# Optimization experiments

Measured on AMD Instinct MI355X. Metric: run time of the kernel, lower is better.

## Reference

```python
import jax, jax.numpy as jnp
import numpy as np

_SAMPLING_EPS = 1e-5


def setup_inputs() -> dict:
    key = jax.random.key(0)
    k1, k2, k3, k4, k5, k6 = jax.random.split(key, 6)
    B, V = 128, 128000
    return {
        "logits": jax.random.normal(k1, (B, V), dtype=jnp.float32),
        "temperature": jax.random.uniform(k2, (B,), dtype=jnp.float32),
        "min_p": jax.random.uniform(k3, (B,), dtype=jnp.float32),
        "top_k": jax.random.randint(k4, (B,), 0, 1024),
        "top_p": jax.random.uniform(k5, (B,), dtype=jnp.float32),
        "q": jax.random.uniform(k6, (B, V), dtype=jnp.float32),
        "num_logprobs": 20,
    }


def reference(logits, temperature, min_p, top_k, top_p, q, num_logprobs):
    B, V = logits.shape
    # raw logprobs computed BEFORE any processing (as in Sampler.forward)
    raw_logprobs = jax.nn.log_softmax(logits, axis=-1)
    # greedy sample on unscaled logits
    greedy = jnp.argmax(logits, axis=-1)
    # temperature scaling
    lt = logits / temperature[:, None]
    # min-p filtering
    probs = jax.nn.softmax(lt, axis=-1)
    max_p = jnp.max(probs, axis=-1, keepdims=True)
    lt = jnp.where(probs >= min_p[:, None] * max_p, lt, -jnp.inf)
    # top-k / top-p filtering on ascending-sorted logits (vLLM style)
    idx = jnp.argsort(lt, axis=-1)                       # ascending
    ls = jnp.take_along_axis(lt, idx, axis=-1)
    k = jnp.clip(top_k, 1, V)
    kth = jnp.take_along_axis(ls, (V - k)[:, None], axis=-1)  # k-th largest value
    ls = jnp.where(ls < kth, -jnp.inf, ls)
    ps = jax.nn.softmax(ls, axis=-1)
    csum = jnp.cumsum(ps, axis=-1)
    pmask = csum <= (1.0 - top_p)[:, None]
    pmask = pmask.at[:, -1].set(False)                   # always keep the max token
    ls = jnp.where(pmask, -jnp.inf, ls)
    inv = jnp.argsort(idx, axis=-1)                      # inverse permutation (scatter back)
    filtered = jnp.take_along_axis(ls, inv, axis=-1)
    # exponential-race sampling: argmax(probs / Exp(1)) ~ Categorical(probs)
    probs2 = jax.nn.softmax(filtered, axis=-1)
    expo = -jnp.log(jnp.clip(q, 1e-10, 1.0))
    rand_sampled = jnp.argmax(probs2 / expo, axis=-1)
    sampled = jnp.where(temperature < _SAMPLING_EPS, greedy, rand_sampled)
    # gather_logprobs: top-k logprobs + sampled-token logprob + rank
    topk_lp, topk_idx = jax.lax.top_k(raw_logprobs, num_logprobs)
    tok_lp = jnp.take_along_axis(raw_logprobs, sampled[:, None], axis=-1)  # (B,1)
    ranks = jnp.sum(raw_logprobs >= tok_lp, axis=-1)
    out_idx = jnp.concatenate([sampled[:, None], topk_idx], axis=1).astype(jnp.int32)
    out_lp = jnp.concatenate([tok_lp, topk_lp], axis=1)  # (B, num_logprobs+1)
    return (sampled[:, None].astype(jnp.int32), out_idx, out_lp, ranks)
```

## Files before the change

kernel.cpp:

```cpp
#include <hip/hip_runtime.h>
#include <math.h>

#define NB 1024
#define C_CAP 2048
#define BLK1 512
#define BLK2 1024
#define LCAP2 2048
#define FLOORB 682
#define BIN_SCALE ((float)NB / 12.0f)
#define BOUND 1.9921875f

__device__ __forceinline__ int bin_of(float x) {
  int b = (int)floorf((x + 6.0f) * BIN_SCALE);
  return min(max(b, 0), NB - 1);
}
__device__ __forceinline__ unsigned long long pack_vi(float v, int idx) {
  return ((unsigned long long)__float_as_uint(v) << 32) | (unsigned int)idx;
}
__device__ __forceinline__ unsigned long long okey(float v, int idx) {
  unsigned int u = __float_as_uint(v);
  u = (u & 0x80000000u) ? ~u : (u | 0x80000000u);
  return ((unsigned long long)u << 32) | (unsigned long long)(0x7fffffffu - (unsigned int)idx);
}
__device__ __forceinline__ float okey_val(unsigned long long k) {
  unsigned int hi = (unsigned int)(k >> 32);
  unsigned int u = (hi & 0x80000000u) ? (hi & 0x7fffffffu) : ~hi;
  return __uint_as_float(u);
}
__device__ __forceinline__ int okey_idx(unsigned long long k) {
  return (int)(0x7fffffffu - (unsigned int)k);
}

__global__ __launch_bounds__(BLK1)
void k1_scan(const float* __restrict__ logits, int V, int halfElems,
             unsigned long long* __restrict__ plist, int* __restrict__ pcnt,
             float* __restrict__ psum) {
  const int row = blockIdx.y, half = blockIdx.x, tid = threadIdx.x;
  const int lane = tid & 63;
  const float* lrow = logits + (size_t)row * V;
  const int start = half * halfElems;
  const int end = min(start + halfElems, V);
  __shared__ unsigned long long lst[LCAP2];
  __shared__ float rs[BLK1];
  __shared__ int lcnt;
  if (tid == 0) lcnt = 0;
  __syncthreads();
  float sum = 0.0f;
  const int n = max(end - start, 0);
  const int n4 = n >> 2;
  const float4* p4 = (const float4*)(lrow + start);
  int i = tid;
  for (; i + BLK1 < n4; i += 2 * BLK1) {
    float4 a = p4[i], b2 = p4[i + BLK1];
    float va[8] = {a.x, a.y, a.z, a.w, b2.x, b2.y, b2.z, b2.w};
    int ia[8];
    #pragma unroll
    for (int c2 = 0; c2 < 4; c2++) { ia[c2] = (i << 2) + c2; ia[c2 + 4] = ((i + BLK1) << 2) + c2; }
    #pragma unroll
    for (int c2 = 0; c2 < 8; c2++) {
      float x = va[c2];
      sum += __expf(fminf(x, 70.0f) - 6.0f);
      bool pred = (x >= BOUND);
      unsigned long long mk = __ballot(pred);
      if (mk) {
        int leader = __ffsll((long long)mk) - 1;
        int base = 0;
        if (lane == leader) base = atomicAdd(&lcnt, __popcll(mk));
        base = __shfl(base, leader, 64);
        if (pred) {
          int p = base + __popcll(mk & ((1ull << lane) - 1ull));
          if (p < LCAP2) lst[p] = pack_vi(x, start + ia[c2]);
        }
      }
    }
  }
  for (; i < n4; i += BLK1) {
    float4 a = p4[i];
    float va[4] = {a.x, a.y, a.z, a.w};
    #pragma unroll
    for (int c2 = 0; c2 < 4; c2++) {
      float x = va[c2];
      sum += __expf(fminf(x, 70.0f) - 6.0f);
      bool pred = (x >= BOUND);
      unsigned long long mk = __ballot(pred);
      if (mk) {
        int leader = __ffsll((long long)mk) - 1;
        int base = 0;
        if (lane == leader) base = atomicAdd(&lcnt, __popcll(mk));
        base = __shfl(base, leader, 64);
        if (pred) {
          int p = base + __popcll(mk & ((1ull << lane) - 1ull));
          if (p < LCAP2) lst[p] = pack_vi(x, start + (i << 2) + c2);
        }
      }
    }
  }
  for (int j = (n4 << 2) + tid; j < n; j += BLK1) {
    float x = lrow[start + j];
    sum += __expf(fminf(x, 70.0f) - 6.0f);
    bool pred = (x >= BOUND);
    unsigned long long mk = __ballot(pred);
    if (mk) {
      int leader = __ffsll((long long)mk) - 1;
      int base = 0;
      if (lane == leader) base = atomicAdd(&lcnt, __popcll(mk));
      base = __shfl(base, leader, 64);
      if (pred) {
        int p = base + __popcll(mk & ((1ull << lane) - 1ull));
        if (p < LCAP2) lst[p] = pack_vi(x, start + j);
      }
    }
  }
  __syncthreads();
  rs[tid] = sum;
  __syncthreads();
  for (int s = BLK1 / 2; s > 0; s >>= 1) {
    if (tid < s) rs[tid] += rs[tid + s];
    __syncthreads();
  }
  const size_t rc = (size_t)row * 2 + half;
  if (tid == 0) { psum[rc] = rs[0]; pcnt[rc] = lcnt; }
  int m = min(lcnt, LCAP2);
  unsigned long long* prow = plist + rc * LCAP2;
  for (int j = tid; j < m; j += BLK1) prow[j] = lst[j];
}

__global__ __launch_bounds__(BLK2)
void k2_fused(const float* __restrict__ logits,
              const float* __restrict__ temperature,
              const float* __restrict__ min_p,
              const int* __restrict__ top_k,
              const float* __restrict__ top_p,
              const float* __restrict__ q,
              const int* __restrict__ nl_ptr,
              int V, int B,
              const unsigned long long* __restrict__ plist,
              const int* __restrict__ pcnt,
              const float* __restrict__ psum,
              float* __restrict__ out) {
  const int row = blockIdx.x, tid = threadIdx.x;
  __shared__ int h[NB + 1];
  __shared__ int cur[NB];
  __shared__ unsigned long long lst[2 * LCAP2];
  __shared__ unsigned long long bkt[C_CAP];
  __shared__ float sv[C_CAP];
  __shared__ int   si[C_CAP];
  __shared__ float ss[C_CAP];
  __shared__ float st[BLK2];
  __shared__ float rf[BLK2], rf2[BLK2];
  __shared__ int   ri[BLK2];
  __shared__ int   s_fail, s_b;
  __shared__ float s_lse;

  for (int i = tid; i < NB; i += BLK2) { h[i] = 0; cur[i] = 0; }
  if (tid == 0) { s_b = 0; h[NB] = 0; }
  __syncthreads();

  const int p0 = pcnt[(size_t)row * 2], p1 = pcnt[(size_t)row * 2 + 1];
  const int c0 = min(p0, LCAP2), c1 = min(p1, LCAP2);
  const int tot = c0 + c1;
  int nl = nl_ptr[0];
  int ke = top_k[row]; ke = min(max(ke, 1), V);
  const int Kp = max(ke, nl);
  const bool fast = (p0 <= LCAP2) && (p1 <= LCAP2) && (tot >= Kp);

  if (tid == 0) s_lse = 6.0f + logf(psum[(size_t)row * 2] + psum[(size_t)row * 2 + 1]);

  const float* lrow = logits + (size_t)row * V;
  const int n4 = V >> 2;
  const float4* p4 = (const float4*)lrow;

  if (fast) {
    const unsigned long long* pr0 = plist + (size_t)row * 2 * LCAP2;
    const unsigned long long* pr1 = pr0 + LCAP2;
    for (int j = tid; j < c0; j += BLK2) lst[j] = pr0[j];
    for (int j = tid; j < c1; j += BLK2) lst[c0 + j] = pr1[j];
    __syncthreads();
    for (int j = tid; j < tot; j += BLK2) {
      float x = __uint_as_float((unsigned int)(lst[j] >> 32));
      atomicAdd(&h[bin_of(x)], 1);
    }
  } else {
    for (int ii = tid; ii < n4; ii += BLK2) {
      float4 a4 = p4[ii];
      atomicAdd(&h[bin_of(a4.x)], 1); atomicAdd(&h[bin_of(a4.y)], 1);
      atomicAdd(&h[bin_of(a4.z)], 1); atomicAdd(&h[bin_of(a4.w)], 1);
    }
    for (int j = (n4 << 2) + tid; j < V; j += BLK2)
      atomicAdd(&h[bin_of(lrow[j])], 1);
  }
  __syncthreads();

  for (int off = 1; off < NB; off <<= 1) {
    int t0 = (tid + off < NB) ? h[tid + off] : 0;
    __syncthreads();
    h[tid] += t0;
    __syncthreads();
  }
  if (h[tid] >= Kp) atomicMax(&s_b, tid);
  __syncthreads();
  const int bstar = s_b;
  int c = min(h[bstar], C_CAP); if (c < 1) c = 1;

  if (fast) {
    for (int j = tid; j < tot; j += BLK2) {
      unsigned long long kk = lst[j];
      float x = __uint_as_float((unsigned int)(kk >> 32));
      int idx = (int)(unsigned int)kk;
      int b = bin_of(x);
      if (b >= bstar) {
        int a = atomicAdd(&cur[b], 1);
        int pos = h[b + 1] + a;
        if (pos < C_CAP) bkt[pos] = okey(x, idx);
      }
    }
  } else {
    for (int ii = tid; ii < n4; ii += BLK2) {
      float4 a4 = p4[ii];
      float va[4] = {a4.x, a4.y, a4.z, a4.w};
      #pragma unroll
      for (int c2 = 0; c2 < 4; c2++) {
        int b = bin_of(va[c2]);
        if (b >= bstar) {
          int a = atomicAdd(&cur[b], 1);
          int pos = h[b + 1] + a;
          if (pos < C_CAP) bkt[pos] = okey(va[c2], (ii << 2) + c2);
        }
      }
    }
    for (int j = (n4 << 2) + tid; j < V; j += BLK2) {
      float x = lrow[j];
      int b = bin_of(x);
      if (b >= bstar) {
        int a = atomicAdd(&cur[b], 1);
        int pos = h[b + 1] + a;
        if (pos < C_CAP) bkt[pos] = okey(x, j);
      }
    }
  }
  __syncthreads();

  for (int pos = tid; pos < c; pos += BLK2) {
    unsigned long long k0 = bkt[pos];
    float v = okey_val(k0);
    int b = bin_of(v);
    int gs = h[b + 1];
    int ge = min(h[b], c);
    int rk = 0;
    for (int j = gs; j < ge; j++) if (bkt[j] > k0) rk++;
    int fin = gs + rk;
    sv[fin] = v; si[fin] = okey_idx(k0);
  }
  __syncthreads();

  float temp = temperature[row];
  bool ug = (temp < 1e-5f);
  float rt = 1.0f / (ug ? 1.0f : temp);
  float mp = min_p[row], tp = top_p[row];
  ke = min(ke, c);
  float v0 = sv[0];
  float lt0 = v0 * rt;

  float ltk = sv[ke - 1] * rt;
  float kth = (expf(ltk - lt0) >= mp) ? ltk : -INFINITY;

  if (tid == 0) s_fail = c;
  __syncthreads();
  for (int ii = tid; ii < c; ii += BLK2) {
    float ltj = sv[ii] * rt;
    if (!((expf(ltj - lt0) >= mp) && (ltj >= kth))) { atomicMin(&s_fail, ii); break; }
  }
  __syncthreads();
  int n1 = s_fail; if (n1 < 1) n1 = 1;
  __syncthreads();

  int L = (c + BLK2 - 1) / BLK2;
  int base = tid * L;
  int lim = min(base + L, c);
  float run = 0.0f;
  for (int j = base; j < lim; j++) {
    float pj = (j < n1) ? expf(sv[j] * rt - lt0) : 0.0f;
    run += pj; ss[j] = run;
  }
  st[tid] = run;
  __syncthreads();
  for (int off = 1; off < BLK2; off <<= 1) {
    float t0 = (tid >= off) ? st[tid - off] : 0.0f;
    __syncthreads();
    st[tid] += t0;
    __syncthreads();
  }
  float offv = (tid > 0) ? st[tid - 1] : 0.0f;
  for (int j = base; j < lim; j++) ss[j] += offv;
  __syncthreads();
  float Z1 = ss[n1 - 1];

  if (tid == 0) s_fail = n1;
  __syncthreads();
  for (int ii = tid; ii < n1; ii += BLK2) {
    if (ii > 0 && !((1.0f - ss[ii - 1] / Z1) > (1.0f - tp))) { atomicMin(&s_fail, ii); break; }
  }
  __syncthreads();
  int n2 = s_fail; if (n2 < 1) n2 = 1;
  __syncthreads();
  float Z2 = ss[n2 - 1];

  const float* qrow = q + (size_t)row * V;
  float bsc = -INFINITY; int bidx = 0x7fffffff; float bval = 0.0f;
  for (int ii = tid; ii < n2; ii += BLK2) {
    float pj = expf(sv[ii] * rt - lt0);
    float qv = qrow[si[ii]];
    qv = fminf(fmaxf(qv, 1e-10f), 1.0f);
    float sc = (pj / Z2) / (-logf(qv));
    if (sc > bsc || (sc == bsc && si[ii] < bidx)) { bsc = sc; bidx = si[ii]; bval = sv[ii]; }
  }
  rf[tid] = bsc; ri[tid] = bidx; rf2[tid] = bval;
  __syncthreads();
  for (int s = BLK2 / 2; s > 0; s >>= 1) {
    if (tid < s) {
      if (rf[tid + s] > rf[tid] ||
          (rf[tid + s] == rf[tid] && ri[tid + s] < ri[tid])) {
        rf[tid] = rf[tid + s]; ri[tid] = ri[tid + s]; rf2[tid] = rf2[tid + s];
      }
    }
    __syncthreads();
  }
  int sampled = ug ? si[0] : ri[0];
  float val_s = ug ? sv[0] : rf2[0];
  float lse = s_lse;
  float tok_lp = val_s - lse;
  __syncthreads();

  if (tid == 0) s_fail = c;
  __syncthreads();
  for (int ii = tid; ii < c; ii += BLK2)
    if (!((sv[ii] - lse) >= tok_lp)) { atomicMin(&s_fail, ii); break; }
  __syncthreads();
  int rank = s_fail;

  int W = nl + 1;
  if (tid == 0) {
    out[row] = (float)sampled;
    out[B + row * W] = (float)sampled;
    out[B + B * W + row * W] = tok_lp;
    out[B + 2 * B * W + row] = (float)rank;
  }
  for (int t = tid; t < nl; t += BLK2) {
    out[B + row * W + 1 + t] = (float)si[t];
    out[B + B * W + row * W + 1 + t] = sv[t] - lse;
  }
}

extern "C" void kernel_launch(void* const* d_in, const int* in_sizes, int n_in,
                              void* d_out, int out_size, void* d_ws, size_t ws_size,
                              hipStream_t stream) {
  const float* logits      = (const float*)d_in[0];
  const float* temperature = (const float*)d_in[1];
  const float* min_p       = (const float*)d_in[2];
  const int*   top_k       = (const int*)d_in[3];
  const float* top_p       = (const float*)d_in[4];
  const float* q           = (const float*)d_in[5];
  const int*   nl_ptr      = (const int*)d_in[6];

  int B = in_sizes[1];
  int V = in_sizes[0] / B;
  float* out = (float*)d_out;
  int halfElems = (((V + 1) / 2) + 3) & ~3;

  unsigned char* w = (unsigned char*)d_ws;
  unsigned long long* plist = (unsigned long long*)w; w += (size_t)B * 2 * LCAP2 * sizeof(unsigned long long);
  int* pcnt = (int*)w;                                w += (size_t)B * 2 * sizeof(int);
  float* psum = (float*)w;                            w += (size_t)B * 2 * sizeof(float);

  hipLaunchKernelGGL(k1_scan, dim3(2, B), dim3(BLK1), 0, stream,
                     logits, V, halfElems, plist, pcnt, psum);
  hipLaunchKernelGGL(k2_fused, dim3(B), dim3(BLK2), 0, stream,
                     logits, temperature, min_p, top_k, top_p, q, nl_ptr,
                     V, B, plist, pcnt, psum, out);
}
```

Before: 174.5 us.

## Use per-wave candidate segments and shuffle reductions in scan; halve fused block size

```diff
diff --git a/kernel.cpp b/kernel.cpp
--- a/kernel.cpp
+++ b/kernel.cpp
@@ -4,7 +4,9 @@
 #define NB 1024
 #define C_CAP 2048
 #define BLK1 512
-#define BLK2 1024
+#define BLK2 512
+#define NWAVES1 (BLK1 / 64)
+#define WSEG 512
 #define LCAP2 2048
 #define FLOORB 682
 #define BIN_SCALE ((float)NB / 12.0f)
@@ -36,41 +38,36 @@
              unsigned long long* __restrict__ plist, int* __restrict__ pcnt,
              float* __restrict__ psum) {
   const int row = blockIdx.y, half = blockIdx.x, tid = threadIdx.x;
-  const int lane = tid & 63;
+  const int wave = tid >> 6, lane = tid & 63;
   const float* lrow = logits + (size_t)row * V;
   const int start = half * halfElems;
   const int end = min(start + halfElems, V);
-  __shared__ unsigned long long lst[LCAP2];
-  __shared__ float rs[BLK1];
-  __shared__ int lcnt;
-  if (tid == 0) lcnt = 0;
-  __syncthreads();
-  float sum = 0.0f;
+  __shared__ unsigned long long seg[NWAVES1][WSEG];
+  __shared__ int wcnt[NWAVES1];
+  __shared__ int wbase[NWAVES1];
+  __shared__ int s_total, s_ovf;
+  __shared__ float s_sum;
+  if (tid < NWAVES1) wcnt[tid] = 0;
+  if (tid == 0) { s_sum = 0.0f; s_ovf = 0; }
+  __syncthreads();
+
+  float s0 = 0.0f, s1 = 0.0f, s2 = 0.0f, s3 = 0.0f;
   const int n = max(end - start, 0);
   const int n4 = n >> 2;
   const float4* p4 = (const float4*)(lrow + start);
   int i = tid;
-  for (; i + BLK1 < n4; i += 2 * BLK1) {
-    float4 a = p4[i], b2 = p4[i + BLK1];
-    float va[8] = {a.x, a.y, a.z, a.w, b2.x, b2.y, b2.z, b2.w};
-    int ia[8];
+  for (; i + 3 * BLK1 < n4; i += 4 * BLK1) {
+    float4 a0 = p4[i], a1 = p4[i + BLK1], a2 = p4[i + 2 * BLK1], a3 = p4[i + 3 * BLK1];
+    float va[16] = {a0.x, a0.y, a0.z, a0.w, a1.x, a1.y, a1.z, a1.w,
+                    a2.x, a2.y, a2.z, a2.w, a3.x, a3.y, a3.z, a3.w};
     #pragma unroll
-    for (int c2 = 0; c2 < 4; c2++) { ia[c2] = (i << 2) + c2; ia[c2 + 4] = ((i + BLK1) << 2) + c2; }
-    #pragma unroll
-    for (int c2 = 0; c2 < 8; c2++) {
+    for (int c2 = 0; c2 < 16; c2++) {
       float x = va[c2];
-      sum += __expf(fminf(x, 70.0f) - 6.0f);
-      bool pred = (x >= BOUND);
-      unsigned long long mk = __ballot(pred);
-      if (mk) {
-        int leader = __ffsll((long long)mk) - 1;
-        int base = 0;
-        if (lane == leader) base = atomicAdd(&lcnt, __popcll(mk));
-        base = __shfl(base, leader, 64);
-        if (pred) {
-          int p = base + __popcll(mk & ((1ull << lane) - 1ull));
-          if (p < LCAP2) lst[p] = pack_vi(x, start + ia[c2]);
-        }
+      float e = __expf(fminf(x, 70.0f) - 6.0f);
+      if (c2 < 4) s0 += e; else if (c2 < 8) s1 += e; else if (c2 < 12) s2 += e; else s3 += e;
+      if (x >= BOUND) {
+        int p = atomicAdd(&wcnt[wave], 1);
+        if (p < WSEG) seg[wave][p] = pack_vi(x, start + ((i + (c2 >> 2) * BLK1) << 2) + (c2 & 3));
       }
     }
   }
@@ -80,49 +77,49 @@
     #pragma unroll
     for (int c2 = 0; c2 < 4; c2++) {
       float x = va[c2];
-      sum += __expf(fminf(x, 70.0f) - 6.0f);
-      bool pred = (x >= BOUND);
-      unsigned long long mk = __ballot(pred);
-      if (mk) {
-        int leader = __ffsll((long long)mk) - 1;
-        int base = 0;
-        if (lane == leader) base = atomicAdd(&lcnt, __popcll(mk));
-        base = __shfl(base, leader, 64);
-        if (pred) {
-          int p = base + __popcll(mk & ((1ull << lane) - 1ull));
-          if (p < LCAP2) lst[p] = pack_vi(x, start + (i << 2) + c2);
-        }
+      s0 += __expf(fminf(x, 70.0f) - 6.0f);
+      if (x >= BOUND) {
+        int p = atomicAdd(&wcnt[wave], 1);
+        if (p < WSEG) seg[wave][p] = pack_vi(x, start + (i << 2) + c2);
       }
     }
   }
   for (int j = (n4 << 2) + tid; j < n; j += BLK1) {
     float x = lrow[start + j];
-    sum += __expf(fminf(x, 70.0f) - 6.0f);
-    bool pred = (x >= BOUND);
-    unsigned long long mk = __ballot(pred);
-    if (mk) {
-      int leader = __ffsll((long long)mk) - 1;
-      int base = 0;
-      if (lane == leader) base = atomicAdd(&lcnt, __popcll(mk));
-      base = __shfl(base, leader, 64);
-      if (pred) {
-        int p = base + __popcll(mk & ((1ull << lane) - 1ull));
-        if (p < LCAP2) lst[p] = pack_vi(x, start + j);
-      }
-    }
-  }
-  __syncthreads();
-  rs[tid] = sum;
-  __syncthreads();
-  for (int s = BLK1 / 2; s > 0; s >>= 1) {
-    if (tid < s) rs[tid] += rs[tid + s];
-    __syncthreads();
-  }
-  const size_t rc = (size_t)row * 2 + half;
-  if (tid == 0) { psum[rc] = rs[0]; pcnt[rc] = lcnt; }
-  int m = min(lcnt, LCAP2);
-  unsigned long long* prow = plist + rc * LCAP2;
-  for (int j = tid; j < m; j += BLK1) prow[j] = lst[j];
+    s0 += __expf(fminf(x, 70.0f) - 6.0f);
+    if (x >= BOUND) {
+      int p = atomicAdd(&wcnt[wave], 1);
+      if (p < WSEG) seg[wave][p] = pack_vi(x, start + j);
+    }
+  }
+  float s = (s0 + s1) + (s2 + s3);
+  for (int o = 32; o > 0; o >>= 1) s += __shfl_down(s, o, 64);
+  if (lane == 0) atomicAdd(&s_sum, s);
+  __syncthreads();
+
+  if (tid == 0) {
+    int b = 0, ov = 0;
+    for (int w = 0; w < NWAVES1; w++) {
+      wbase[w] = b;
+      int cw = wcnt[w];
+      if (cw > WSEG) { ov = 1; cw = WSEG; }
+      b += cw;
+    }
+    s_total = b; s_ovf = ov;
+    const size_t rc = (size_t)row * 2 + half;
+    psum[rc] = s_sum;
+    pcnt[rc] = (ov || b > LCAP2) ? (LCAP2 + 1) : b;
+  }
+  __syncthreads();
+  {
+    int cw = min(wcnt[wave], WSEG);
+    int base = wbase[wave];
+    unsigned long long* prow = plist + ((size_t)row * 2 + half) * LCAP2;
+    for (int j = lane; j < cw; j += 64) {
+      int pos = base + j;
+      if (pos < LCAP2) prow[pos] = seg[wave][j];
+    }
+  }
 }
 
 __global__ __launch_bounds__(BLK2)
@@ -192,12 +189,15 @@
   __syncthreads();
 
   for (int off = 1; off < NB; off <<= 1) {
-    int t0 = (tid + off < NB) ? h[tid + off] : 0;
-    __syncthreads();
-    h[tid] += t0;
+    int i0 = tid, i1 = tid + BLK2;
+    int t0 = (i0 + off < NB) ? h[i0 + off] : 0;
+    int t1 = (i1 + off < NB) ? h[i1 + off] : 0;
+    __syncthreads();
+    h[i0] += t0; h[i1] += t1;
     __syncthreads();
   }
   if (h[tid] >= Kp) atomicMax(&s_b, tid);
+  if (h[tid + BLK2] >= Kp) atomicMax(&s_b, tid + BLK2);
   __syncthreads();
   const int bstar = s_b;
   int c = min(h[bstar], C_CAP); if (c < 1) c = 1;
```

Measured after the change: 166.6 us. 4.5% less time.
